# Kernel tuning notes

Measured on AMD Instinct MI355X. Metric: run time of the kernel, lower is better.

Reference implementation:

```python
import jax, jax.numpy as jnp
import numpy as np

NUM_USERS = 100000
USER_EMB_DIM = 64
PROC_DIM = 128          # Dense(128) embedding_processor
NUM_SHARDS = 16
MEM_SIZE = 512          # memory slots per shard
WORD_SIZE = 64
NUM_READS = 4
INPUT_SIZE = 256
B, S = 256, 128
IN_DIM = INPUT_SIZE + PROC_DIM  # combined controller input width


def setup_inputs() -> dict:
    key = jax.random.key(0)
    k = jax.random.split(key, 7)
    x = jax.random.normal(k[0], (B, S, INPUT_SIZE), dtype=jnp.float32)
    user_id = jax.random.randint(k[1], (B,), 0, NUM_USERS, dtype=jnp.int64)
    user_emb_table = jax.random.normal(k[2], (NUM_USERS, USER_EMB_DIM), dtype=jnp.float32) * 0.02
    W_proc = jax.random.normal(k[3], (USER_EMB_DIM, PROC_DIM), dtype=jnp.float32) * (1.0 / np.sqrt(USER_EMB_DIM))
    b_proc = jnp.zeros((PROC_DIM,), dtype=jnp.float32)
    # per-shard parameters: query projection + memory matrix (the shard's state)
    Wq = jax.random.normal(k[4], (NUM_SHARDS, IN_DIM, NUM_READS * WORD_SIZE), dtype=jnp.float32) * (1.0 / np.sqrt(IN_DIM))
    memory = jax.random.normal(k[5], (NUM_SHARDS, MEM_SIZE, WORD_SIZE), dtype=jnp.float32)
    return {"x": x, "user_id": user_id, "user_emb_table": user_emb_table,
            "W_proc": W_proc, "b_proc": b_proc, "Wq": Wq, "memory": memory}


def reference(x, user_id, user_emb_table, W_proc, b_proc, Wq, memory):
    # user embedding lookup + Dense processor
    ue = user_emb_table[user_id]                       # [B, E]
    pe = ue @ W_proc + b_proc                          # [B, PROC_DIM]
    # broadcast the processed embedding across the sequence and concat on features
    pe_seq = jnp.broadcast_to(pe[:, None, :], (x.shape[0], x.shape[1], pe.shape[-1]))
    combined = jnp.concatenate([x, pe_seq], axis=-1)   # [B, S, IN_DIM]
    # shard routing (irregular gather of per-shard params)
    sid = user_id % NUM_SHARDS                         # [B]
    Wq_g = Wq[sid]                                     # [B, IN_DIM, R*W]
    mem_g = memory[sid]                                # [B, M, W]
    # per-sample shard forward: content-based read
    q = jnp.einsum('bsi,bio->bso', combined, Wq_g)     # [B, S, R*W]
    q = q.reshape(q.shape[0], q.shape[1], NUM_READS, WORD_SIZE)
    scores = jnp.einsum('bsrw,bmw->bsrm', q, mem_g)    # [B, S, R, M]
    wts = jax.nn.softmax(scores, axis=-1)
    read_words = jnp.einsum('bsrm,bmw->bsrw', wts, mem_g)  # [B, S, R, W]
    # original code keeps final_states[-1] (last sample's state)
    final_state = wts[-1]                              # [S, R, M]
    return read_words, final_state
```

## Files before the change

### kernel.cpp

```cpp
#include <hip/hip_runtime.h>
#include <math.h>

#define BB 256
#define SSEQ 128
#define INPUT 256
#define PD 128
#define EE 64
#define RW 256
#define MM 512
#define WW 64
#define KD 384

typedef _Float16 half8 __attribute__((ext_vector_type(8)));
typedef __fp16 fp16x2 __attribute__((ext_vector_type(2)));
typedef float float4v __attribute__((ext_vector_type(4)));
typedef float f32x16 __attribute__((ext_vector_type(16)));
typedef unsigned int uint2v __attribute__((ext_vector_type(2)));

#define LOG2E 1.44269504088896f
#define OUT1 8388608u

#define MEMT_OFF 65536
#define MEMT16   4096
#define F32_OFF  131072
#define LDS_BYTES (131072 + 6144)
#define UE_O 0
#define PE_O 64
#define QPE_O 192
#define QP_O 448

union H8 { half8 h8; unsigned int u[4]; uint4 u4; };

__device__ __forceinline__ unsigned int pk2(float a, float b) {
    union { fp16x2 h; unsigned int u; } p;
    p.h = __builtin_amdgcn_cvt_pkrtz(a, b);
    return p.u;
}

__device__ __forceinline__ float xhalf_max(float v) {
    uint2v r = __builtin_amdgcn_permlane32_swap(__float_as_uint(v), __float_as_uint(v), false, false);
    return fmaxf(__uint_as_float(r[0]), __uint_as_float(r[1]));
}
__device__ __forceinline__ float xhalf_sum(float v) {
    uint2v r = __builtin_amdgcn_permlane32_swap(__float_as_uint(v), __float_as_uint(v), false, false);
    return __uint_as_float(r[0]) + __uint_as_float(r[1]);
}

__global__ void __launch_bounds__(1024, 4)
attn_kernel(const float* __restrict__ x, const int* __restrict__ user_id,
            const float* __restrict__ uet, const float* __restrict__ W_proc,
            const float* __restrict__ b_proc, const float* __restrict__ Wq,
            const float* __restrict__ memG, float* __restrict__ out)
{
    extern __shared__ char smraw[];
    unsigned short* smemu = (unsigned short*)smraw;
    unsigned int*   smw   = (unsigned int*)smraw;
    uint4*          sm128 = (uint4*)smraw;
    float*          smf   = (float*)(smraw + F32_OFF);

    const int t = threadIdx.x;
    const int b = blockIdx.x;
    const int lane = t & 63, wv = t >> 6;
    const int n16 = lane & 15, quad = lane >> 4;
    const int l31 = lane & 31, hh = lane >> 5;
    const int r = wv & 3, sq = wv >> 2;
    const int s0 = sq * 32;
    const int mswz = l31 & 7;

    const int uid = user_id[b];
    const int sid = uid & 15;
    const float* memB = memG + (size_t)sid * (MM*WW);
    const float* wqX  = Wq + (size_t)sid * KD * RW;

    if (t < EE) smf[UE_O + t] = uet[(size_t)uid*EE + t];

    for (int i = 0; i < 32; ++i) {
        int idx = i*1024 + t;
        int n = idx & 255, kp = idx >> 8;
        float w0 = wqX[(size_t)(2*kp)    *RW + n];
        float w1 = wqX[(size_t)(2*kp + 1)*RW + n];
        smw[((((kp>>2)*256 + n) << 2) | (kp & 3))] = pk2(w0, w1);
    }
    __syncthreads();

    if (t < PD) {
        float a = b_proc[t];
        #pragma unroll
        for (int e = 0; e < EE; ++e) a = fmaf(smf[UE_O + e], W_proc[e*PD + t], a);
        smf[PE_O + t] = a;
    }
    __syncthreads();
    {
        int n = t & 255, h = t >> 8;
        float s = 0.f;
        const float* wr = wqX + (size_t)(256 + h*32)*RW + n;
        #pragma unroll 8
        for (int k = 0; k < 32; ++k) s = fmaf(smf[PE_O + h*32 + k], wr[(size_t)k*RW], s);
        smf[QP_O + h*256 + n] = s;
    }
    __syncthreads();
    if (t < 256) smf[QPE_O + t] = LOG2E * (smf[QP_O + t] + smf[QP_O + 256 + t]
                                         + smf[QP_O + 512 + t] + smf[QP_O + 768 + t]);
    __syncthreads();

    float4v qacc[4][2];
    #pragma unroll
    for (int mt = 0; mt < 4; ++mt)
        #pragma unroll
        for (int nt = 0; nt < 2; ++nt) qacc[mt][nt] = (float4v)0.f;

    const float* xB = x + (size_t)(b*SSEQ + s0) * INPUT;
    for (int kc = 0; kc < 8; ++kc) {
        H8 afr[4];
        #pragma unroll
        for (int mt = 0; mt < 4; ++mt)
            afr[mt].u4 = sm128[(kc*4 + quad)*256 + r*64 + mt*16 + n16];
        H8 bfr[2];
        #pragma unroll
        for (int nt = 0; nt < 2; ++nt) {
            const float* xg = xB + (size_t)(nt*16 + n16)*INPUT + kc*32 + quad*8;
            float4 a0 = *(const float4*)xg;
            float4 a1 = *(const float4*)(xg + 4);
            bfr[nt].u[0] = pk2(a0.x*LOG2E, a0.y*LOG2E);
            bfr[nt].u[1] = pk2(a0.z*LOG2E, a0.w*LOG2E);
            bfr[nt].u[2] = pk2(a1.x*LOG2E, a1.y*LOG2E);
            bfr[nt].u[3] = pk2(a1.z*LOG2E, a1.w*LOG2E);
        }
        #pragma unroll
        for (int mt = 0; mt < 4; ++mt)
            #pragma unroll
            for (int nt = 0; nt < 2; ++nt)
                qacc[mt][nt] = __builtin_amdgcn_mfma_f32_16x16x32_f16(afr[mt].h8, bfr[nt].h8, qacc[mt][nt], 0, 0, 0);
    }
    #pragma unroll
    for (int mt = 0; mt < 4; ++mt)
        #pragma unroll
        for (int reg = 0; reg < 4; ++reg) {
            float qv = smf[QPE_O + r*64 + mt*16 + quad*4 + reg];
            #pragma unroll
            for (int nt = 0; nt < 2; ++nt) qacc[mt][nt][reg] += qv;
        }
    unsigned int pkq[4][2][2];
    #pragma unroll
    for (int mt = 0; mt < 4; ++mt)
        #pragma unroll
        for (int nt = 0; nt < 2; ++nt) {
            pkq[mt][nt][0] = pk2(qacc[mt][nt][0], qacc[mt][nt][1]);
            pkq[mt][nt][1] = pk2(qacc[mt][nt][2], qacc[mt][nt][3]);
        }
    H8 bqf[4];
    {
        const int ntSel = (lane >> 4) & 1;
        const int srcBase = (lane & 15) + (lane & 32);
        #pragma unroll
        for (int kc = 0; kc < 4; ++kc)
            #pragma unroll
            for (int jp = 0; jp < 4; ++jp) {
                const int src = srcBase + ((jp >> 1) << 4);
                int v0 = __shfl((int)pkq[kc][0][jp & 1], src, 64);
                int v1 = __shfl((int)pkq[kc][1][jp & 1], src, 64);
                bqf[kc].u[jp] = (unsigned int)(ntSel ? v1 : v0);
            }
    }
    __syncthreads();

    for (int i = 0; i < 4; ++i) {
        int id = t + i*1024;
        int m = id >> 3, cw = id & 7;
        const float* g = memB + m*64 + cw*8;
        float4 a0 = *(const float4*)g;
        float4 a1 = *(const float4*)(g + 4);
        sm128[m*8 + (cw ^ (m & 7))] =
            make_uint4(pk2(a0.x,a0.y), pk2(a0.z,a0.w), pk2(a1.x,a1.y), pk2(a1.z,a1.w));
    }
    __syncthreads();
    for (int i = 0; i < 4; ++i) {
        int id = t + i*1024;
        int w = id & 63, cm = id >> 6;
        unsigned int uu[4];
        #pragma unroll
        for (int p = 0; p < 4; ++p) {
            int m0 = cm*8 + 2*p, m1 = m0 + 1;
            unsigned short lo = smemu[m0*64 + (((w>>3) ^ (m0&7))<<3) + (w&7)];
            unsigned short hi = smemu[m1*64 + (((w>>3) ^ (m1&7))<<3) + (w&7)];
            uu[p] = (unsigned int)lo | ((unsigned int)hi << 16);
        }
        sm128[MEMT16 + w*64 + (cm ^ (w & 7))] = make_uint4(uu[0],uu[1],uu[2],uu[3]);
    }
    __syncthreads();

    f32x16 Oa0 = (f32x16)0.f, Oa1 = (f32x16)0.f;
    float Ml = -1e30f, llp = 0.f;

    for (int mtile = 0; mtile < 16; ++mtile) {
        f32x16 Sa = (f32x16)0.f;
        const int mrow = mtile*32 + l31;
        #pragma unroll
        for (int kc = 0; kc < 4; ++kc) {
            H8 af; af.u4 = sm128[mrow*8 + (((kc<<1) + hh) ^ mswz)];
            Sa = __builtin_amdgcn_mfma_f32_32x32x16_f16(af.h8, bqf[kc].h8, Sa, 0, 0, 0);
        }
        float tma = fmaxf(fmaxf(fmaxf(Sa[0],Sa[1]), fmaxf(Sa[2],Sa[3])),
                          fmaxf(fmaxf(Sa[4],Sa[5]), fmaxf(Sa[6],Sa[7])));
        float tmb = fmaxf(fmaxf(fmaxf(Sa[8],Sa[9]), fmaxf(Sa[10],Sa[11])),
                          fmaxf(fmaxf(Sa[12],Sa[13]), fmaxf(Sa[14],Sa[15])));
        float tm = xhalf_max(fmaxf(tma, tmb));
        float Mn = fmaxf(Ml, tm);
        float al = __builtin_amdgcn_exp2f(Ml - Mn);
        float pv[16];
        #pragma unroll
        for (int g = 0; g < 16; ++g) pv[g] = __builtin_amdgcn_exp2f(Sa[g] - Mn);
        float ts = (((pv[0]+pv[1])+(pv[2]+pv[3])) + ((pv[4]+pv[5])+(pv[6]+pv[7])))
                 + (((pv[8]+pv[9])+(pv[10]+pv[11])) + ((pv[12]+pv[13])+(pv[14]+pv[15])));
        llp = al*llp + ts;
        Ml = Mn;
        #pragma unroll
        for (int g = 0; g < 16; ++g) { Oa0[g] *= al; Oa1[g] *= al; }
        uint2v rA0 = __builtin_amdgcn_permlane32_swap(pk2(pv[0],pv[1]),   pk2(pv[4],pv[5]),   false, false);
        uint2v rB0 = __builtin_amdgcn_permlane32_swap(pk2(pv[2],pv[3]),   pk2(pv[6],pv[7]),   false, false);
        uint2v rA1 = __builtin_amdgcn_permlane32_swap(pk2(pv[8],pv[9]),   pk2(pv[12],pv[13]), false, false);
        uint2v rB1 = __builtin_amdgcn_permlane32_swap(pk2(pv[10],pv[11]), pk2(pv[14],pv[15]), false, false);
        H8 bp0; bp0.u[0]=rA0[0]; bp0.u[1]=rB0[0]; bp0.u[2]=rA0[1]; bp0.u[3]=rB0[1];
        H8 bp1; bp1.u[0]=rA1[0]; bp1.u[1]=rB1[0]; bp1.u[2]=rA1[1]; bp1.u[3]=rB1[1];
        const int c0 = mtile*4 + hh;
        {
            H8 af0; af0.u4 = sm128[MEMT16 + l31*64        + ( c0      ^ mswz)];
            Oa0 = __builtin_amdgcn_mfma_f32_32x32x16_f16(af0.h8, bp0.h8, Oa0, 0, 0, 0);
            H8 af1; af1.u4 = sm128[MEMT16 + l31*64        + ((c0 + 2) ^ mswz)];
            Oa0 = __builtin_amdgcn_mfma_f32_32x32x16_f16(af1.h8, bp1.h8, Oa0, 0, 0, 0);
            H8 af2; af2.u4 = sm128[MEMT16 + (32 + l31)*64 + ( c0      ^ mswz)];
            Oa1 = __builtin_amdgcn_mfma_f32_32x32x16_f16(af2.h8, bp0.h8, Oa1, 0, 0, 0);
            H8 af3; af3.u4 = sm128[MEMT16 + (32 + l31)*64 + ((c0 + 2) ^ mswz)];
            Oa1 = __builtin_amdgcn_mfma_f32_32x32x16_f16(af3.h8, bp1.h8, Oa1, 0, 0, 0);
        }
    }

    float inv = 1.0f / xhalf_sum(llp);

    {
        const int s = s0 + l31;
        float* op = out + ((size_t)(b*SSEQ + s)*4 + r)*WW;
        #pragma unroll
        for (int rq = 0; rq < 4; ++rq) {
            float4 o0 = make_float4(Oa0[rq*4+0]*inv, Oa0[rq*4+1]*inv,
                                    Oa0[rq*4+2]*inv, Oa0[rq*4+3]*inv);
            *(float4*)&op[rq*8 + hh*4] = o0;
            float4 o1 = make_float4(Oa1[rq*4+0]*inv, Oa1[rq*4+1]*inv,
                                    Oa1[rq*4+2]*inv, Oa1[rq*4+3]*inv);
            *(float4*)&op[32 + rq*8 + hh*4] = o1;
        }
    }

    if (b == BB - 1) {
        const int s = s0 + l31;
        size_t base = (size_t)OUT1 + ((size_t)(s*4 + r) << 9);
        for (int mtile = 0; mtile < 16; ++mtile) {
            f32x16 Sa = (f32x16)0.f;
            const int mrow = mtile*32 + l31;
            #pragma unroll
            for (int kc = 0; kc < 4; ++kc) {
                H8 af; af.u4 = sm128[mrow*8 + (((kc<<1) + hh) ^ mswz)];
                Sa = __builtin_amdgcn_mfma_f32_32x32x16_f16(af.h8, bqf[kc].h8, Sa, 0, 0, 0);
            }
            #pragma unroll
            for (int rq = 0; rq < 4; ++rq) {
                float4 w4 = make_float4(
                    __builtin_amdgcn_exp2f(Sa[rq*4+0] - Ml) * inv,
                    __builtin_amdgcn_exp2f(Sa[rq*4+1] - Ml) * inv,
                    __builtin_amdgcn_exp2f(Sa[rq*4+2] - Ml) * inv,
                    __builtin_amdgcn_exp2f(Sa[rq*4+3] - Ml) * inv);
                *(float4*)&out[base + mtile*32 + rq*8 + hh*4] = w4;
            }
        }
    }
}

extern "C" void kernel_launch(void* const* d_in, const int* in_sizes, int n_in,
                              void* d_out, int out_size, void* d_ws, size_t ws_size,
                              hipStream_t stream) {
    const float* x    = (const float*)d_in[0];
    const int*   uid  = (const int*)  d_in[1];
    const float* uet  = (const float*)d_in[2];
    const float* Wp   = (const float*)d_in[3];
    const float* bp   = (const float*)d_in[4];
    const float* Wq   = (const float*)d_in[5];
    const float* mem  = (const float*)d_in[6];
    float* out = (float*)d_out;

    (void)hipFuncSetAttribute((const void*)attn_kernel,
                              hipFuncAttributeMaxDynamicSharedMemorySize, LDS_BYTES);
    attn_kernel<<<BB, 1024, LDS_BYTES, stream>>>(x, uid, uet, Wp, bp, Wq, mem, out);
}
```

Before: 164.8 us.

## Prefetch LDS fragments, lazily rescale softmax, and raise priority around MFMAs

Double-buffers the memory-tile A fragments for the score MFMAs and issues the read-side LDS loads before the softmax math, so LDS latency overlaps with compute. The online softmax now rescales the running max and accumulators only when some lane's tile max exceeds the running max by more than a threshold, skipping most rescale multiplies and exp calls. s_setprio is raised around MFMA groups to favour matrix issue across waves. The lazy rescale lets exponentials grow up to 2^8 before rescaling, which adds fp16 overflow risk for pv values; the prefetch raises register pressure.

```diff
diff --git a/kernel.cpp b/kernel.cpp
--- a/kernel.cpp
+++ b/kernel.cpp
@@ -126,11 +126,13 @@
             bfr[nt].u[2] = pk2(a1.x*LOG2E, a1.y*LOG2E);
             bfr[nt].u[3] = pk2(a1.z*LOG2E, a1.w*LOG2E);
         }
+        __builtin_amdgcn_s_setprio(1);
         #pragma unroll
         for (int mt = 0; mt < 4; ++mt)
             #pragma unroll
             for (int nt = 0; nt < 2; ++nt)
                 qacc[mt][nt] = __builtin_amdgcn_mfma_f32_16x16x32_f16(afr[mt].h8, bfr[nt].h8, qacc[mt][nt], 0, 0, 0);
+        __builtin_amdgcn_s_setprio(0);
     }
     #pragma unroll
     for (int mt = 0; mt < 4; ++mt)
@@ -192,47 +194,64 @@
     f32x16 Oa0 = (f32x16)0.f, Oa1 = (f32x16)0.f;
     float Ml = -1e30f, llp = 0.f;
 
+    H8 afc[4];
+    #pragma unroll
+    for (int kc = 0; kc < 4; ++kc)
+        afc[kc].u4 = sm128[l31*8 + (((kc<<1) + hh) ^ mswz)];
+
     for (int mtile = 0; mtile < 16; ++mtile) {
         f32x16 Sa = (f32x16)0.f;
-        const int mrow = mtile*32 + l31;
-        #pragma unroll
-        for (int kc = 0; kc < 4; ++kc) {
-            H8 af; af.u4 = sm128[mrow*8 + (((kc<<1) + hh) ^ mswz)];
-            Sa = __builtin_amdgcn_mfma_f32_32x32x16_f16(af.h8, bqf[kc].h8, Sa, 0, 0, 0);
-        }
-        float tma = fmaxf(fmaxf(fmaxf(Sa[0],Sa[1]), fmaxf(Sa[2],Sa[3])),
-                          fmaxf(fmaxf(Sa[4],Sa[5]), fmaxf(Sa[6],Sa[7])));
-        float tmb = fmaxf(fmaxf(fmaxf(Sa[8],Sa[9]), fmaxf(Sa[10],Sa[11])),
-                          fmaxf(fmaxf(Sa[12],Sa[13]), fmaxf(Sa[14],Sa[15])));
-        float tm = xhalf_max(fmaxf(tma, tmb));
-        float Mn = fmaxf(Ml, tm);
-        float al = __builtin_amdgcn_exp2f(Ml - Mn);
+        __builtin_amdgcn_s_setprio(1);
+        #pragma unroll
+        for (int kc = 0; kc < 4; ++kc)
+            Sa = __builtin_amdgcn_mfma_f32_32x32x16_f16(afc[kc].h8, bqf[kc].h8, Sa, 0, 0, 0);
+        __builtin_amdgcn_s_setprio(0);
+        if (mtile < 15) {
+            const int mrow = (mtile+1)*32 + l31;
+            #pragma unroll
+            for (int kc = 0; kc < 4; ++kc)
+                afc[kc].u4 = sm128[mrow*8 + (((kc<<1) + hh) ^ mswz)];
+        }
+        const int c0 = mtile*4 + hh;
+        H8 afP0, afP1, afP2, afP3;
+        afP0.u4 = sm128[MEMT16 + l31*64        + ( c0      ^ mswz)];
+        afP1.u4 = sm128[MEMT16 + l31*64        + ((c0 + 2) ^ mswz)];
+        afP2.u4 = sm128[MEMT16 + (32 + l31)*64 + ( c0      ^ mswz)];
+        afP3.u4 = sm128[MEMT16 + (32 + l31)*64 + ((c0 + 2) ^ mswz)];
+        float m0 = fmaxf(fmaxf(Sa[0], Sa[1]), Sa[2]);
+        float m1 = fmaxf(fmaxf(Sa[3], Sa[4]), Sa[5]);
+        float m2 = fmaxf(fmaxf(Sa[6], Sa[7]), Sa[8]);
+        float m3 = fmaxf(fmaxf(Sa[9], Sa[10]), Sa[11]);
+        float m4 = fmaxf(fmaxf(Sa[12], Sa[13]), Sa[14]);
+        float m5 = fmaxf(fmaxf(m0, m1), Sa[15]);
+        float m6 = fmaxf(fmaxf(m2, m3), m4);
+        float tmx = xhalf_max(fmaxf(m5, m6));
+        if (__any(tmx > Ml + 8.0f)) {
+            float Mn = fmaxf(Ml, tmx);
+            float al = __builtin_amdgcn_exp2f(Ml - Mn);
+            Ml = Mn;
+            llp *= al;
+            #pragma unroll
+            for (int g = 0; g < 16; ++g) { Oa0[g] *= al; Oa1[g] *= al; }
+        }
         float pv[16];
         #pragma unroll
-        for (int g = 0; g < 16; ++g) pv[g] = __builtin_amdgcn_exp2f(Sa[g] - Mn);
+        for (int g = 0; g < 16; ++g) pv[g] = __builtin_amdgcn_exp2f(Sa[g] - Ml);
         float ts = (((pv[0]+pv[1])+(pv[2]+pv[3])) + ((pv[4]+pv[5])+(pv[6]+pv[7])))
                  + (((pv[8]+pv[9])+(pv[10]+pv[11])) + ((pv[12]+pv[13])+(pv[14]+pv[15])));
-        llp = al*llp + ts;
-        Ml = Mn;
-        #pragma unroll
-        for (int g = 0; g < 16; ++g) { Oa0[g] *= al; Oa1[g] *= al; }
+        llp += ts;
         uint2v rA0 = __builtin_amdgcn_permlane32_swap(pk2(pv[0],pv[1]),   pk2(pv[4],pv[5]),   false, false);
         uint2v rB0 = __builtin_amdgcn_permlane32_swap(pk2(pv[2],pv[3]),   pk2(pv[6],pv[7]),   false, false);
         uint2v rA1 = __builtin_amdgcn_permlane32_swap(pk2(pv[8],pv[9]),   pk2(pv[12],pv[13]), false, false);
         uint2v rB1 = __builtin_amdgcn_permlane32_swap(pk2(pv[10],pv[11]), pk2(pv[14],pv[15]), false, false);
         H8 bp0; bp0.u[0]=rA0[0]; bp0.u[1]=rB0[0]; bp0.u[2]=rA0[1]; bp0.u[3]=rB0[1];
         H8 bp1; bp1.u[0]=rA1[0]; bp1.u[1]=rB1[0]; bp1.u[2]=rA1[1]; bp1.u[3]=rB1[1];
-        const int c0 = mtile*4 + hh;
-        {
-            H8 af0; af0.u4 = sm128[MEMT16 + l31*64        + ( c0      ^ mswz)];
-            Oa0 = __builtin_amdgcn_mfma_f32_32x32x16_f16(af0.h8, bp0.h8, Oa0, 0, 0, 0);
-            H8 af1; af1.u4 = sm128[MEMT16 + l31*64        + ((c0 + 2) ^ mswz)];
-            Oa0 = __builtin_amdgcn_mfma_f32_32x32x16_f16(af1.h8, bp1.h8, Oa0, 0, 0, 0);
-            H8 af2; af2.u4 = sm128[MEMT16 + (32 + l31)*64 + ( c0      ^ mswz)];
-            Oa1 = __builtin_amdgcn_mfma_f32_32x32x16_f16(af2.h8, bp0.h8, Oa1, 0, 0, 0);
-            H8 af3; af3.u4 = sm128[MEMT16 + (32 + l31)*64 + ((c0 + 2) ^ mswz)];
-            Oa1 = __builtin_amdgcn_mfma_f32_32x32x16_f16(af3.h8, bp1.h8, Oa1, 0, 0, 0);
-        }
+        __builtin_amdgcn_s_setprio(1);
+        Oa0 = __builtin_amdgcn_mfma_f32_32x32x16_f16(afP0.h8, bp0.h8, Oa0, 0, 0, 0);
+        Oa0 = __builtin_amdgcn_mfma_f32_32x32x16_f16(afP1.h8, bp1.h8, Oa0, 0, 0, 0);
+        Oa1 = __builtin_amdgcn_mfma_f32_32x32x16_f16(afP2.h8, bp0.h8, Oa1, 0, 0, 0);
+        Oa1 = __builtin_amdgcn_mfma_f32_32x32x16_f16(afP3.h8, bp1.h8, Oa1, 0, 0, 0);
+        __builtin_amdgcn_s_setprio(0);
     }
 
     float inv = 1.0f / xhalf_sum(llp);
```

New measurement: 165.8 us. Within noise of the previous version (+0.6%).
